# Kernel optimization log

Measured on AMD Instinct MI355X. Metric: run time of the kernel, lower is better.

The kernel has to match this reference:

```python
import jax, jax.numpy as jnp
import numpy as np

B, N, H = 2, 160, 256
F = 512  # num_hidden_fc
C3 = 3 * H  # concatenated modality feature
C6 = 2 * C3  # pairwise feature


def setup_inputs() -> dict:
    key = jax.random.key(0)
    ks = jax.random.split(key, 16)
    s1 = 1.0 / np.sqrt(C6)
    s2 = 1.0 / np.sqrt(F)
    inp = {
        "geometry": jax.random.normal(ks[0], (B, N, H), jnp.float32),
        "appearance": jax.random.normal(ks[1], (B, N, H), jnp.float32),
        "content": jax.random.normal(ks[2], (B, N, H), jnp.float32),
    }
    for i, name in enumerate(["cell", "row", "col"]):
        inp[f"{name}_W1"] = jax.random.normal(ks[3 + 4 * i], (C6, F), jnp.float32) * s1
        inp[f"{name}_b1"] = jnp.zeros((F,), jnp.float32)
        inp[f"{name}_W2"] = jax.random.normal(ks[4 + 4 * i], (F, 2), jnp.float32) * s2
        inp[f"{name}_b2"] = jnp.zeros((2,), jnp.float32)
    return inp


def _head(x, W1, b1, W2, b2):
    h = jax.nn.relu(jnp.einsum("bpc,cf->bpf", x, W1) + b1)
    return jax.nn.softmax(jnp.einsum("bpf,fk->bpk", h, W2) + b2, axis=-1)


def reference(geometry, appearance, content,
              cell_W1, cell_b1, cell_W2, cell_b2,
              row_W1, row_b1, row_W2, row_b2,
              col_W1, col_b1, col_W2, col_b2):
    emb = jnp.concatenate([geometry, appearance, content], axis=-1)  # (B,N,3H)
    b, n, c = emb.shape
    # pairs[b,i,j] = concat(emb[b,j], emb[b,i])  (matches unsqueeze(1)/unsqueeze(2) order)
    e_j = jnp.broadcast_to(emb[:, None, :, :], (b, n, n, c))
    e_i = jnp.broadcast_to(emb[:, :, None, :], (b, n, n, c))
    emb_pairs = jnp.concatenate([e_j, e_i], axis=-1).reshape(b, n * n, 2 * c)
    cell_logits = _head(emb_pairs, cell_W1, cell_b1, cell_W2, cell_b2)
    row_logits = _head(emb_pairs, row_W1, row_b1, row_W2, row_b2)
    col_logits = _head(emb_pairs, col_W1, col_b1, col_W2, col_b2)
    return cell_logits, row_logits, col_logits, emb_pairs
```

## Files before the change

kernel.cpp:

```cpp
#include <hip/hip_runtime.h>

#define NB 2
#define NN 160
#define NPAIR (NN*NN)
#define OUT_PAIRS_OFF 307200

__global__ __launch_bounds__(256) void proj_fp32_kernel(
    const float* __restrict__ geo, const float* __restrict__ app,
    const float* __restrict__ con,
    const float* __restrict__ w1c, const float* __restrict__ w1r,
    const float* __restrict__ w1l,
    const float* __restrict__ b1c, const float* __restrict__ b1r,
    const float* __restrict__ b1l,
    float* __restrict__ proj)
{
    __shared__ float As[64][17];
    __shared__ float Bs[16][68];

    const int tid = threadIdx.x;
    const int m0 = blockIdx.x * 64;
    const int n0 = blockIdx.y * 64;
    const int t  = n0 >> 10;
    const int s  = (n0 >> 9) & 1;
    const int f0 = n0 & 511;

    const float* w1 = (t == 0) ? w1c : ((t == 1) ? w1r : w1l);
    const float* b1 = (t == 0) ? b1c : ((t == 1) ? b1r : b1l);

    const int ty = tid >> 4, tx = tid & 15;
    const int ar = tid >> 2, ac = (tid & 3) * 4;
    const int bk = tid >> 4, bn = (tid & 15) * 4;

    float acc[4][4] = {};

    for (int k0 = 0; k0 < 768; k0 += 16) {
        {
            const int c = k0 + ac;
            const int m = c >> 8, off = c & 255;
            const float* src = ((m == 0) ? geo : (m == 1) ? app : con)
                               + (size_t)(m0 + ar) * 256 + off;
            const float4 v = *(const float4*)src;
            As[ar][ac + 0] = v.x; As[ar][ac + 1] = v.y;
            As[ar][ac + 2] = v.z; As[ar][ac + 3] = v.w;
        }
        {
            const float4 v = *(const float4*)(
                w1 + (size_t)(s * 768 + k0 + bk) * 512 + f0 + bn);
            Bs[bk][bn + 0] = v.x; Bs[bk][bn + 1] = v.y;
            Bs[bk][bn + 2] = v.z; Bs[bk][bn + 3] = v.w;
        }
        __syncthreads();

        #pragma unroll
        for (int k = 0; k < 16; ++k) {
            const float4 b = *(const float4*)&Bs[k][tx * 4];
            const float a0 = As[ty * 4 + 0][k];
            const float a1 = As[ty * 4 + 1][k];
            const float a2 = As[ty * 4 + 2][k];
            const float a3 = As[ty * 4 + 3][k];
            acc[0][0] += a0 * b.x; acc[0][1] += a0 * b.y;
            acc[0][2] += a0 * b.z; acc[0][3] += a0 * b.w;
            acc[1][0] += a1 * b.x; acc[1][1] += a1 * b.y;
            acc[1][2] += a1 * b.z; acc[1][3] += a1 * b.w;
            acc[2][0] += a2 * b.x; acc[2][1] += a2 * b.y;
            acc[2][2] += a2 * b.z; acc[2][3] += a2 * b.w;
            acc[3][0] += a3 * b.x; acc[3][1] += a3 * b.y;
            acc[3][2] += a3 * b.z; acc[3][3] += a3 * b.w;
        }
        __syncthreads();
    }

    float4 bias = {0.f, 0.f, 0.f, 0.f};
    if (s == 0) bias = *(const float4*)&b1[f0 + tx * 4];

    #pragma unroll
    for (int r = 0; r < 4; ++r) {
        float4 o;
        o.x = acc[r][0] + bias.x; o.y = acc[r][1] + bias.y;
        o.z = acc[r][2] + bias.z; o.w = acc[r][3] + bias.w;
        *(float4*)&proj[(size_t)((t * 2 + s) * 320 + m0 + ty * 4 + r) * 512
                        + f0 + tx * 4] = o;
    }
}

__global__ __launch_bounds__(64) void heads_kernel(
    const float* __restrict__ proj,
    const float* __restrict__ w2c, const float* __restrict__ b2c,
    const float* __restrict__ w2r, const float* __restrict__ b2r,
    const float* __restrict__ w2l, const float* __restrict__ b2l,
    float* __restrict__ out)
{
    __shared__ float P1s[8][516];
    __shared__ float P2s[8][516];
    __shared__ float w2s[1024];
    __shared__ float b2s[2];

    const int tid = threadIdx.x;
    const int bid = blockIdx.x;
    const int b   = bid / 400;
    const int rem = bid - b * 400;
    const int it  = rem / 20;
    const int jt  = rem - it * 20;
    const int i0 = it * 8, j0 = jt * 8;
    const int ii = tid >> 3, jj = tid & 7;

    #pragma unroll
    for (int t = 0; t < 3; ++t) {
        const float* w2 = (t == 0) ? w2c : ((t == 1) ? w2r : w2l);
        const float* b2 = (t == 0) ? b2c : ((t == 1) ? b2r : b2l);

        for (int u = tid; u < 2048; u += 64) {
            const int tile = u >> 10;
            const int r    = (u >> 7) & 7;
            const int f4   = u & 127;
            const int p    = b * 160 + (tile ? (i0 + r) : (j0 + r));
            const float4 v = *(const float4*)(
                proj + ((size_t)((t * 2 + tile) * 320 + p)) * 512 + f4 * 4);
            float* dst = tile ? &P2s[r][f4 * 4] : &P1s[r][f4 * 4];
            *(float4*)dst = v;
        }
        for (int u = tid; u < 256; u += 64)
            *(float4*)&w2s[u * 4] = *(const float4*)(w2 + u * 4);
        if (tid < 2) b2s[tid] = b2[tid];
        __syncthreads();

        float a0 = b2s[0], a1 = b2s[1];
        for (int f = 0; f < 512; f += 4) {
            const float4 p1 = *(const float4*)&P1s[jj][f];
            const float4 p2 = *(const float4*)&P2s[ii][f];
            const float4 wA = *(const float4*)&w2s[f * 2];
            const float4 wB = *(const float4*)&w2s[f * 2 + 4];
            const float h0 = fmaxf(p1.x + p2.x, 0.f);
            const float h1 = fmaxf(p1.y + p2.y, 0.f);
            const float h2 = fmaxf(p1.z + p2.z, 0.f);
            const float h3 = fmaxf(p1.w + p2.w, 0.f);
            a0 += h0 * wA.x + h1 * wA.z + h2 * wB.x + h3 * wB.z;
            a1 += h0 * wA.y + h1 * wA.w + h2 * wB.y + h3 * wB.w;
        }

        const float mx = fmaxf(a0, a1);
        const float e0 = __expf(a0 - mx);
        const float e1 = __expf(a1 - mx);
        const float rs = 1.f / (e0 + e1);

        const int pr = b * 25600 + (i0 + ii) * 160 + (j0 + jj);
        float2 o; o.x = e0 * rs; o.y = e1 * rs;
        ((float2*)out)[t * 51200 + pr] = o;
        __syncthreads();
    }
}

__global__ __launch_bounds__(256) void pairs_kernel(
    const float* __restrict__ geo, const float* __restrict__ app,
    const float* __restrict__ con,
    float4* __restrict__ outp)
{
    const int idx = blockIdx.x * 256 + threadIdx.x;
    const int row = idx / 384;
    const int c   = idx - row * 384;
    const int b   = row / 25600;
    const int rem = row - b * 25600;
    const int i   = rem / 160;
    const int j   = rem - i * 160;

    int cc = c, pt = j;
    if (c >= 192) { pt = i; cc = c - 192; }
    const int m   = cc >> 6;
    const int off = cc & 63;
    const float* src = ((m == 0) ? geo : (m == 1) ? app : con)
                       + ((size_t)(b * 160 + pt)) * 256 + off * 4;

    outp[idx] = *(const float4*)src;
}

extern "C" void kernel_launch(void* const* d_in, const int* in_sizes, int n_in,
                              void* d_out, int out_size, void* d_ws, size_t ws_size,
                              hipStream_t stream)
{
    const float* geo = (const float*)d_in[0];
    const float* app = (const float*)d_in[1];
    const float* con = (const float*)d_in[2];
    const float* w1c = (const float*)d_in[3];
    const float* b1c = (const float*)d_in[4];
    const float* w2c = (const float*)d_in[5];
    const float* b2c = (const float*)d_in[6];
    const float* w1r = (const float*)d_in[7];
    const float* b1r = (const float*)d_in[8];
    const float* w2r = (const float*)d_in[9];
    const float* b2r = (const float*)d_in[10];
    const float* w1l = (const float*)d_in[11];
    const float* b1l = (const float*)d_in[12];
    const float* w2l = (const float*)d_in[13];
    const float* b2l = (const float*)d_in[14];

    float* out = (float*)d_out;

    float* proj = out + OUT_PAIRS_OFF;

    proj_fp32_kernel<<<dim3(5, 48), 256, 0, stream>>>(
        geo, app, con, w1c, w1r, w1l, b1c, b1r, b1l, proj);

    heads_kernel<<<800, 64, 0, stream>>>(
        proj, w2c, b2c, w2r, b2r, w2l, b2l, out);

    pairs_kernel<<<76800, 256, 0, stream>>>(
        geo, app, con, (float4*)(out + OUT_PAIRS_OFF));
}
```

Measured before the change: 447.2 us.

## Overlap pair-broadcast writes with projection and head kernels via block splitting

```diff
diff --git a/kernel.cpp b/kernel.cpp
--- a/kernel.cpp
+++ b/kernel.cpp
@@ -5,21 +5,58 @@
 #define NPAIR (NN*NN)
 #define OUT_PAIRS_OFF 307200
 
-__global__ __launch_bounds__(256) void proj_fp32_kernel(
+#define TOTAL_CHUNKS 19660800
+#define TAIL_CHUNKS 245760
+#define TAIL_START (TOTAL_CHUNKS - TAIL_CHUNKS)
+#define PROJ_SCRATCH_OFF (OUT_PAIRS_OFF + 4*TAIL_START)
+
+#define K1_PAIR_BLOCKS 42240
+#define S1_CHUNKS (K1_PAIR_BLOCKS*256)
+#define K2_PAIR_BLOCKS 33600
+
+__device__ __forceinline__ void pairs_chunk(
+    const float* __restrict__ geo, const float* __restrict__ app,
+    const float* __restrict__ con, float4* __restrict__ outp, int idx)
+{
+    const int row = idx / 384;
+    const int c   = idx - row * 384;
+    const int b   = row / 25600;
+    const int rem = row - b * 25600;
+    const int i   = rem / 160;
+    const int j   = rem - i * 160;
+
+    int cc = c, pt = j;
+    if (c >= 192) { pt = i; cc = c - 192; }
+    const int m   = cc >> 6;
+    const int off = cc & 63;
+    const float* src = ((m == 0) ? geo : (m == 1) ? app : con)
+                       + ((size_t)(b * 160 + pt)) * 256 + off * 4;
+
+    outp[idx] = *(const float4*)src;
+}
+
+__global__ __launch_bounds__(256) void k1_proj_pairs(
     const float* __restrict__ geo, const float* __restrict__ app,
     const float* __restrict__ con,
     const float* __restrict__ w1c, const float* __restrict__ w1r,
     const float* __restrict__ w1l,
     const float* __restrict__ b1c, const float* __restrict__ b1r,
     const float* __restrict__ b1l,
-    float* __restrict__ proj)
-{
+    float* __restrict__ proj, float4* __restrict__ outp)
+{
+    const int tid = threadIdx.x;
+    const int bid = blockIdx.x;
+
+    if (bid >= 240) {
+        pairs_chunk(geo, app, con, outp, (bid - 240) * 256 + tid);
+        return;
+    }
+
     __shared__ float As[64][17];
     __shared__ float Bs[16][68];
 
-    const int tid = threadIdx.x;
-    const int m0 = blockIdx.x * 64;
-    const int n0 = blockIdx.y * 64;
+    const int m0 = (bid % 5) * 64;
+    const int n0 = (bid / 5) * 64;
     const int t  = n0 >> 10;
     const int s  = (n0 >> 9) & 1;
     const int f0 = n0 & 511;
@@ -83,35 +120,44 @@
     }
 }
 
-__global__ __launch_bounds__(64) void heads_kernel(
+__global__ __launch_bounds__(256) void k2_heads_pairs(
+    const float* __restrict__ geo, const float* __restrict__ app,
+    const float* __restrict__ con,
     const float* __restrict__ proj,
     const float* __restrict__ w2c, const float* __restrict__ b2c,
     const float* __restrict__ w2r, const float* __restrict__ b2r,
     const float* __restrict__ w2l, const float* __restrict__ b2l,
-    float* __restrict__ out)
-{
-    __shared__ float P1s[8][516];
-    __shared__ float P2s[8][516];
+    float* __restrict__ out, float4* __restrict__ outp)
+{
+    const int tid = threadIdx.x;
+    const int bid = blockIdx.x;
+
+    if (bid >= 200) {
+        pairs_chunk(geo, app, con, outp,
+                    S1_CHUNKS + (bid - 200) * 256 + tid);
+        return;
+    }
+
+    __shared__ float P1s[16][516];
+    __shared__ float P2s[16][516];
     __shared__ float w2s[1024];
     __shared__ float b2s[2];
 
-    const int tid = threadIdx.x;
-    const int bid = blockIdx.x;
-    const int b   = bid / 400;
-    const int rem = bid - b * 400;
-    const int it  = rem / 20;
-    const int jt  = rem - it * 20;
-    const int i0 = it * 8, j0 = jt * 8;
-    const int ii = tid >> 3, jj = tid & 7;
+    const int b   = bid / 100;
+    const int rem = bid - b * 100;
+    const int it  = rem / 10;
+    const int jt  = rem - it * 10;
+    const int i0 = it * 16, j0 = jt * 16;
+    const int ii = tid >> 4, jj = tid & 15;
 
     #pragma unroll
     for (int t = 0; t < 3; ++t) {
         const float* w2 = (t == 0) ? w2c : ((t == 1) ? w2r : w2l);
         const float* b2 = (t == 0) ? b2c : ((t == 1) ? b2r : b2l);
 
-        for (int u = tid; u < 2048; u += 64) {
-            const int tile = u >> 10;
-            const int r    = (u >> 7) & 7;
+        for (int u = tid; u < 4096; u += 256) {
+            const int tile = u >> 11;
+            const int r    = (u >> 7) & 15;
             const int f4   = u & 127;
             const int p    = b * 160 + (tile ? (i0 + r) : (j0 + r));
             const float4 v = *(const float4*)(
@@ -119,8 +165,8 @@
             float* dst = tile ? &P2s[r][f4 * 4] : &P1s[r][f4 * 4];
             *(float4*)dst = v;
         }
-        for (int u = tid; u < 256; u += 64)
-            *(float4*)&w2s[u * 4] = *(const float4*)(w2 + u * 4);
+        if (tid < 256)
+            *(float4*)&w2s[tid * 4] = *(const float4*)(w2 + tid * 4);
         if (tid < 2) b2s[tid] = b2[tid];
         __syncthreads();
 
@@ -150,27 +196,12 @@
     }
 }
 
-__global__ __launch_bounds__(256) void pairs_kernel(
-    const float* __restrict__ geo, const float* __restrict__ app,
-    const float* __restrict__ con,
-    float4* __restrict__ outp)
-{
-    const int idx = blockIdx.x * 256 + threadIdx.x;
-    const int row = idx / 384;
-    const int c   = idx - row * 384;
-    const int b   = row / 25600;
-    const int rem = row - b * 25600;
-    const int i   = rem / 160;
-    const int j   = rem - i * 160;
-
-    int cc = c, pt = j;
-    if (c >= 192) { pt = i; cc = c - 192; }
-    const int m   = cc >> 6;
-    const int off = cc & 63;
-    const float* src = ((m == 0) ? geo : (m == 1) ? app : con)
-                       + ((size_t)(b * 160 + pt)) * 256 + off * 4;
-
-    outp[idx] = *(const float4*)src;
+__global__ __launch_bounds__(256) void k3_pairs_tail(
+    const float* __restrict__ geo, const float* __restrict__ app,
+    const float* __restrict__ con, float4* __restrict__ outp)
+{
+    pairs_chunk(geo, app, con, outp,
+                TAIL_START + blockIdx.x * 256 + threadIdx.x);
 }
 
 extern "C" void kernel_launch(void* const* d_in, const int* in_sizes, int n_in,
@@ -195,14 +226,14 @@
 
     float* out = (float*)d_out;
 
-    float* proj = out + OUT_PAIRS_OFF;
-
-    proj_fp32_kernel<<<dim3(5, 48), 256, 0, stream>>>(
-        geo, app, con, w1c, w1r, w1l, b1c, b1r, b1l, proj);
-
-    heads_kernel<<<800, 64, 0, stream>>>(
-        proj, w2c, b2c, w2r, b2r, w2l, b2l, out);
-
-    pairs_kernel<<<76800, 256, 0, stream>>>(
-        geo, app, con, (float4*)(out + OUT_PAIRS_OFF));
-}
+    float* proj = out + PROJ_SCRATCH_OFF;
+    float4* outp = (float4*)(out + OUT_PAIRS_OFF);
+
+    k1_proj_pairs<<<240 + K1_PAIR_BLOCKS, 256, 0, stream>>>(
+        geo, app, con, w1c, w1r, w1l, b1c, b1r, b1l, proj, outp);
+
+    k2_heads_pairs<<<200 + K2_PAIR_BLOCKS, 256, 0, stream>>>(
+        geo, app, con, proj, w2c, b2c, w2r, b2r, w2l, b2l, out, outp);
+
+    k3_pairs_tail<<<960, 256, 0, stream>>>(geo, app, con, outp);
+}
```

New measurement: 429.5 us. 4.0% less time.
